# Optimization experiments

Measured on AMD Instinct MI355X. Metric: run time of the kernel, lower is better.

## Reference

```python
import jax, jax.numpy as jnp
import numpy as np

D_MODEL, D_FF, R, N_ADAPTERS = 1024, 4096, 8, 4


def setup_inputs() -> dict:
    key = jax.random.key(0)
    ks = jax.random.split(key, 8)
    s1 = 1.0 / np.sqrt(D_MODEL)
    s2 = 1.0 / np.sqrt(D_FF)
    x = jax.random.normal(ks[0], (4, 4096, D_MODEL), dtype=jnp.float32)
    w1 = jax.random.uniform(ks[1], (D_MODEL, D_FF), jnp.float32, -s1, s1)
    b1 = jax.random.uniform(ks[2], (D_FF,), jnp.float32, -s1, s1)
    w2 = jax.random.uniform(ks[3], (D_FF, D_MODEL), jnp.float32, -s2, s2)
    b2 = jax.random.uniform(ks[4], (D_MODEL,), jnp.float32, -s2, s2)
    # stacked adapters: down [A, d_model, r], up [A, r, d_model] (no bias)
    a_down = jax.random.uniform(ks[5], (N_ADAPTERS, D_MODEL, R), jnp.float32, -s1, s1)
    a_up = jax.random.uniform(ks[6], (N_ADAPTERS, R, D_MODEL), jnp.float32, -1.0 / np.sqrt(R), 1.0 / np.sqrt(R))
    return {"x": x, "w1": w1, "b1": b1, "w2": w2, "b2": b2,
            "a_down": a_down, "a_up": a_up, "adapter_idx": 0}


def reference(x, w1, b1, w2, b2, a_down, a_up, adapter_idx):
    # FFN: gelu(x @ w1 + b1) @ w2 + b2  (torch F.gelu default = exact erf form)
    h = jax.nn.gelu(jnp.einsum('bsd,df->bsf', x, w1) + b1, approximate=False)
    out = jnp.einsum('bsf,fd->bsd', h, w2) + b2
    # low-rank adapter residual: (x @ A_down) @ A_up
    lora = jnp.einsum('bsd,dr->bsr', x, a_down[adapter_idx])
    out = out + jnp.einsum('bsr,rd->bsd', lora, a_up[adapter_idx])
    return out
```

## Files before the change

### kernel.cpp

```cpp
#include <hip/hip_runtime.h>
#include <hip/hip_bf16.h>
#include <math.h>

typedef __attribute__((ext_vector_type(4))) float floatx4;
typedef __attribute__((ext_vector_type(8))) __bf16 bfloatx8;
typedef __attribute__((ext_vector_type(8))) unsigned short ushortx8;

static __device__ __forceinline__ unsigned short f2bf(float f) {
  __hip_bfloat16 h = __float2bfloat16(f);
  return *reinterpret_cast<unsigned short*>(&h);
}

static __device__ __forceinline__ void gload16(const void* g, void* l) {
  __builtin_amdgcn_global_load_lds(
      (const __attribute__((address_space(1))) unsigned int*)g,
      (__attribute__((address_space(3))) unsigned int*)l, 16, 0, 0);
}

#define S_BARRIER() __builtin_amdgcn_s_barrier()
#define WAIT_VM(n)  do { asm volatile("s_waitcnt vmcnt(" #n ")" ::: "memory"); __builtin_amdgcn_sched_barrier(0); } while (0)

__global__ __launch_bounds__(256) void transpose_bf16_kernel(const float* __restrict__ in,
                                                             unsigned short* __restrict__ out,
                                                             int rows, int cols) {
  __shared__ float tile[32][33];
  int c0 = blockIdx.x * 32, r0 = blockIdx.y * 32;
  int tx = threadIdx.x, ty = threadIdx.y;
#pragma unroll
  for (int j = 0; j < 32; j += 8)
    tile[ty + j][tx] = in[(size_t)(r0 + ty + j) * cols + c0 + tx];
  __syncthreads();
#pragma unroll
  for (int j = 0; j < 32; j += 8)
    out[(size_t)(c0 + ty + j) * rows + r0 + tx] = f2bf(tile[tx][ty + j]);
}

__global__ __launch_bounds__(256) void lora_mid_convert_kernel(const float* __restrict__ x,
                                                               const float* __restrict__ a_down,
                                                               const int* __restrict__ idxp,
                                                               float* __restrict__ lmid,
                                                               unsigned short* __restrict__ Xb) {
  __shared__ float ad[1024 * 9];
  const float* A = a_down + (size_t)(*idxp) * (1024 * 8);
  int t = threadIdx.x;
  for (int i = t; i < 2048; i += 256) {
    float4 v = ((const float4*)A)[i];
    int row = i >> 1, p = (i & 1) * 4;
    ad[row * 9 + p] = v.x; ad[row * 9 + p + 1] = v.y;
    ad[row * 9 + p + 2] = v.z; ad[row * 9 + p + 3] = v.w;
  }
  __syncthreads();
  int wid = t >> 6, lane = t & 63;
  int row = blockIdx.x * 4 + wid;
  const float4* xr4 = (const float4*)(x + (size_t)row * 1024);
  ushort4* xbr4 = (ushort4*)(Xb + (size_t)row * 1024);
  float acc[8] = {0.f, 0.f, 0.f, 0.f, 0.f, 0.f, 0.f, 0.f};
#pragma unroll
  for (int c = 0; c < 4; ++c) {
    int i4 = c * 64 + lane;
    float4 xv = xr4[i4];
    ushort4 o;
    o.x = f2bf(xv.x); o.y = f2bf(xv.y); o.z = f2bf(xv.z); o.w = f2bf(xv.w);
    xbr4[i4] = o;
    const int kb = i4 * 4;
    const float xs[4] = {xv.x, xv.y, xv.z, xv.w};
#pragma unroll
    for (int j = 0; j < 4; ++j)
#pragma unroll
      for (int r = 0; r < 8; ++r) acc[r] += xs[j] * ad[(kb + j) * 9 + r];
  }
#pragma unroll
  for (int off = 32; off > 0; off >>= 1) {
#pragma unroll
    for (int r = 0; r < 8; ++r) acc[r] += __shfl_xor(acc[r], off);
  }
  if (lane == 0) {
    *(float4*)(lmid + (size_t)row * 8) = make_float4(acc[0], acc[1], acc[2], acc[3]);
    *(float4*)(lmid + (size_t)row * 8 + 4) = make_float4(acc[4], acc[5], acc[6], acc[7]);
  }
}

template <int LD, int NKT>
static __device__ __forceinline__ void gemm_kloop3(const unsigned short* __restrict__ A,
                                                   const unsigned short* __restrict__ B,
                                                   size_t m0, size_t n0, char* smem,
                                                   floatx4 (&acc)[4][4]) {
  const int t = threadIdx.x;
  const int wid = t >> 6, lane = t & 63;
  const int wr = wid >> 1, wc = wid & 1;
  const int lr = lane & 15, kg = lane >> 4;
  const int kgx = kg ^ ((lr >> 1) & 3);
  const int srow = t >> 2, scol = ((t & 3) ^ ((t >> 3) & 3)) * 8;
  const unsigned short* gA0 = A + (m0 + srow) * LD + scol;
  const unsigned short* gA1 = A + (m0 + 64 + srow) * LD + scol;
  const unsigned short* gB0 = B + (n0 + srow) * LD + scol;
  const unsigned short* gB1 = B + (n0 + 64 + srow) * LD + scol;
  const unsigned ldsOff = (unsigned)(wid << 10);

#define STAGE(bufb, ko)                           \
  do {                                            \
    char* lA_ = smem + (bufb) + ldsOff;           \
    char* lB_ = smem + (bufb) + 8192 + ldsOff;    \
    gload16(gA0 + (ko), lA_);                     \
    gload16(gA1 + (ko), lA_ + 4096);              \
    gload16(gB0 + (ko), lB_);                     \
    gload16(gB1 + (ko), lB_ + 4096);              \
  } while (0)

  STAGE(0u, 0);
  STAGE(16384u, 32);
  WAIT_VM(4);
  S_BARRIER();

  unsigned cur = 0u, stg = 32768u;
#pragma unroll 1
  for (int kt = 0; kt < NKT; ++kt) {
    if (kt + 2 < NKT) STAGE(stg, (kt + 2) * 32);
    const unsigned short* As = (const unsigned short*)(smem + cur);
    const unsigned short* Bs = (const unsigned short*)(smem + cur + 8192);
    bfloatx8 af[4], bfv[4];
#pragma unroll
    for (int mi = 0; mi < 4; ++mi)
      af[mi] = *(const bfloatx8*)(As + (wr * 64 + mi * 16 + lr) * 32 + kgx * 8);
#pragma unroll
    for (int ni = 0; ni < 4; ++ni)
      bfv[ni] = *(const bfloatx8*)(Bs + (wc * 64 + ni * 16 + lr) * 32 + kgx * 8);
#pragma unroll
    for (int mi = 0; mi < 4; ++mi) {
#pragma unroll
      for (int ni = 0; ni < 4; ++ni)
        acc[mi][ni] = __builtin_amdgcn_mfma_f32_16x16x32_bf16(af[mi], bfv[ni], acc[mi][ni], 0, 0, 0);
    }
    if (kt + 2 < NKT) { WAIT_VM(4); } else { WAIT_VM(0); }
    S_BARRIER();
    cur = (cur == 32768u) ? 0u : cur + 16384u;
    stg = (stg == 32768u) ? 0u : stg + 16384u;
  }
#undef STAGE
}

__global__ __launch_bounds__(256, 3) void gemm1_gelu_kernel(const unsigned short* __restrict__ A,
                                                            const unsigned short* __restrict__ B,
                                                            const float* __restrict__ bias,
                                                            unsigned short* __restrict__ H) {
  __shared__ __align__(16) char smem[49152];
  const int t = threadIdx.x;
  const int wid = t >> 6, lane = t & 63;
  const int wr = wid >> 1, wc = wid & 1;
  const int lr = lane & 15, kg = lane >> 4;

  const int bid = blockIdx.x;
  const int xcd = bid & 7, j = bid >> 3;
  const int sq = j >> 6, i = j & 63;
  const int mt = xcd * 16 + (sq & 1) * 8 + (i & 7);
  const int nt = (sq >> 1) * 8 + (i >> 3);
  const size_t m0 = (size_t)mt * 128;
  const size_t n0 = (size_t)nt * 128;

  floatx4 acc[4][4] = {};
  gemm_kloop3<1024, 32>(A, B, m0, n0, smem, acc);

  __syncthreads();
  float* sE = (float*)smem;
  const int row32 = t >> 3, col0 = (t & 7) * 16;
  const int stripe = row32 >> 4, lrow = row32 & 15;
#pragma unroll
  for (int mi = 0; mi < 4; ++mi) {
#pragma unroll
    for (int ni = 0; ni < 4; ++ni) {
#pragma unroll
      for (int r = 0; r < 4; ++r)
        sE[wr * 2048 + (kg * 4 + r) * 128 + wc * 64 + ni * 16 + lr] = acc[mi][ni][r];
    }
    __syncthreads();
    const size_t gm = m0 + stripe * 64 + mi * 16 + lrow;
    const float* src = sE + stripe * 2048 + lrow * 128 + col0;
    alignas(16) unsigned short pk[16];
#pragma unroll
    for (int i2 = 0; i2 < 16; ++i2) {
      float v = src[i2] + bias[n0 + col0 + i2];
      float g = 0.5f * v * (1.0f + erff(v * 0.70710678118654752440f));
      pk[i2] = f2bf(g);
    }
    *(ushortx8*)(H + gm * 4096 + n0 + col0) = *(const ushortx8*)&pk[0];
    *(ushortx8*)(H + gm * 4096 + n0 + col0 + 8) = *(const ushortx8*)&pk[8];
    __syncthreads();
  }
}

__global__ __launch_bounds__(512) void gemm2_out_kernel(const unsigned short* __restrict__ A,
                                                        const unsigned short* __restrict__ B,
                                                        const float* __restrict__ bias,
                                                        const float* __restrict__ lmid,
                                                        const float* __restrict__ a_up,
                                                        const int* __restrict__ idxp,
                                                        float* __restrict__ OUT) {
  extern __shared__ char smem[];
  const int t = threadIdx.x;
  const int w = t >> 6, lane = t & 63, lr = lane & 15, kg = lane >> 4;
  const int kgx = kg ^ ((lr >> 1) & 3);
  constexpr int LD = 4096, NKT = 128;

  const int bid = blockIdx.x;
  const int xcd = bid & 7, j = bid >> 3;
  const size_t m0 = (size_t)(xcd * 8 + (j >> 3)) * 256;
  const size_t n0 = (size_t)(j & 7) * 128;

  const int sr = w * 16 + (lane >> 2);
  const int scol = ((t & 3) ^ ((sr >> 1) & 3)) * 8;
  const unsigned short* gA0 = A + (m0 + sr) * LD + scol;
  const unsigned short* gA1 = A + (m0 + 128 + sr) * LD + scol;
  const unsigned short* gB = B + (n0 + sr) * LD + scol;
  const unsigned wOff = (unsigned)(w << 10);

#define STAGE2(bufb, ko)                              \
  do {                                                \
    gload16(gA0 + (ko), smem + (bufb) + wOff);        \
    gload16(gA1 + (ko), smem + (bufb) + 8192 + wOff); \
    gload16(gB + (ko), smem + (bufb) + 16384 + wOff); \
  } while (0)

  floatx4 acc[2][8] = {};

  STAGE2(0u, 0);
  STAGE2(24576u, 32);
  WAIT_VM(3);
  S_BARRIER();

  unsigned cur = 0u, stg = 49152u;
#pragma unroll 1
  for (int kt = 0; kt < NKT; ++kt) {
    if (kt + 2 < NKT) STAGE2(stg, (kt + 2) * 32);
    const unsigned short* As = (const unsigned short*)(smem + cur);
    const unsigned short* Bs = (const unsigned short*)(smem + cur + 16384);
    bfloatx8 af[2];
#pragma unroll
    for (int mi = 0; mi < 2; ++mi)
      af[mi] = *(const bfloatx8*)(As + (unsigned)(w * 32 + mi * 16 + lr) * 32 + (unsigned)kgx * 8);
    {
      bfloatx8 bfA[4];
#pragma unroll
      for (int ni = 0; ni < 4; ++ni)
        bfA[ni] = *(const bfloatx8*)(Bs + (unsigned)(ni * 16 + lr) * 32 + (unsigned)kgx * 8);
#pragma unroll
      for (int mi = 0; mi < 2; ++mi)
#pragma unroll
        for (int ni = 0; ni < 4; ++ni)
          acc[mi][ni] = __builtin_amdgcn_mfma_f32_16x16x32_bf16(af[mi], bfA[ni], acc[mi][ni], 0, 0, 0);
    }
    {
      bfloatx8 bfB[4];
#pragma unroll
      for (int ni = 0; ni < 4; ++ni)
        bfB[ni] = *(const bfloatx8*)(Bs + (unsigned)((ni + 4) * 16 + lr) * 32 + (unsigned)kgx * 8);
#pragma unroll
      for (int mi = 0; mi < 2; ++mi)
#pragma unroll
        for (int ni = 0; ni < 4; ++ni)
          acc[mi][4 + ni] = __builtin_amdgcn_mfma_f32_16x16x32_bf16(af[mi], bfB[ni], acc[mi][4 + ni], 0, 0, 0);
    }
    if (kt + 2 < NKT) { WAIT_VM(3); } else { WAIT_VM(0); }
    S_BARRIER();
    cur = (cur == 49152u) ? 0u : cur + 24576u;
    stg = (stg == 49152u) ? 0u : stg + 24576u;
  }
#undef STAGE2

  __syncthreads();
  float* sE = (float*)smem;
  const float* aup = a_up + (size_t)(*idxp) * 8192;
  const int erow = t >> 3, ec0 = (t & 7) * 16;
#pragma unroll
  for (int mi = 0; mi < 2; ++mi) {
#pragma unroll
    for (int ni = 0; ni < 8; ++ni)
#pragma unroll
      for (int r = 0; r < 4; ++r)
        sE[(w * 16 + kg * 4 + r) * 128 + ni * 16 + lr] = acc[mi][ni][r];
    __syncthreads();
#pragma unroll
    for (int h = 0; h < 2; ++h) {
      const int row = erow + h * 64;
      const size_t gm = m0 + (size_t)(row >> 4) * 32 + mi * 16 + (row & 15);
      const int gc = (int)n0 + ec0;
      const float* src = sE + row * 128 + ec0;
      alignas(16) float lmv[8];
      *(float4*)&lmv[0] = *(const float4*)(lmid + gm * 8);
      *(float4*)&lmv[4] = *(const float4*)(lmid + gm * 8 + 4);
      alignas(16) float v[16];
#pragma unroll
      for (int i2 = 0; i2 < 16; ++i2) v[i2] = src[i2] + bias[gc + i2];
#pragma unroll
      for (int r = 0; r < 8; ++r) {
        const float lw = lmv[r];
        const float* ar = aup + r * 1024 + gc;
#pragma unroll
        for (int i2 = 0; i2 < 16; ++i2) v[i2] += lw * ar[i2];
      }
#pragma unroll
      for (int i2 = 0; i2 < 16; i2 += 4)
        *(float4*)(OUT + gm * 1024 + gc + i2) = *(const float4*)&v[i2];
    }
    __syncthreads();
  }
}

extern "C" void kernel_launch(void* const* d_in, const int* in_sizes, int n_in,
                              void* d_out, int out_size, void* d_ws, size_t ws_size,
                              hipStream_t stream) {
  const float* x      = (const float*)d_in[0];
  const float* w1     = (const float*)d_in[1];
  const float* b1     = (const float*)d_in[2];
  const float* w2     = (const float*)d_in[3];
  const float* b2     = (const float*)d_in[4];
  const float* a_down = (const float*)d_in[5];
  const float* a_up   = (const float*)d_in[6];
  const int*   idx    = (const int*)d_in[7];
  float* out = (float*)d_out;

  char* ws = (char*)d_ws;
  unsigned short* Xb  = (unsigned short*)(ws);
  unsigned short* W1T = (unsigned short*)(ws + 33554432);
  unsigned short* W2T = (unsigned short*)(ws + 41943040);
  float*          LMID = (float*)(ws + 50331648);
  unsigned short* H   = (unsigned short*)(ws + 50855936);

  (void)hipFuncSetAttribute((const void*)gemm2_out_kernel, hipFuncAttributeMaxDynamicSharedMemorySize, 73728);

  transpose_bf16_kernel<<<dim3(128, 32), dim3(32, 8), 0, stream>>>(w1, W1T, 1024, 4096);
  transpose_bf16_kernel<<<dim3(32, 128), dim3(32, 8), 0, stream>>>(w2, W2T, 4096, 1024);
  lora_mid_convert_kernel<<<4096, 256, 0, stream>>>(x, a_down, idx, LMID, Xb);
  gemm1_gelu_kernel<<<4096, 256, 0, stream>>>(Xb, W1T, b1, H);
  gemm2_out_kernel<<<512, 512, 73728, stream>>>(H, W2T, b2, LMID, a_up, idx, out);
}
```

Baseline: 441.3 us.

## Enlarge GEMM1 tile to 256x128 with 512 threads and 8 waves

The first GEMM goes from 128x128 tiles with 256 threads and 48KB static LDS to 256x128 tiles with 512 threads (8 waves, each owning 32 rows by 128 columns) and 72KB dynamic LDS in a triple-buffered pipeline. The grid halves to 2048 blocks and the bias+GELU epilogue is remapped to the new layout. The aim is more operand reuse per LDS byte and fewer B-tile loads from global memory. In exchange, register pressure rises and occupancy falls, since fewer blocks fit per CU.

```diff
diff --git a/kernel.cpp b/kernel.cpp
--- a/kernel.cpp
+++ b/kernel.cpp
@@ -80,110 +80,110 @@
   }
 }
 
-template <int LD, int NKT>
-static __device__ __forceinline__ void gemm_kloop3(const unsigned short* __restrict__ A,
-                                                   const unsigned short* __restrict__ B,
-                                                   size_t m0, size_t n0, char* smem,
-                                                   floatx4 (&acc)[4][4]) {
+
+__global__ __launch_bounds__(512) void gemm1_gelu_kernel(const unsigned short* __restrict__ A,
+                                                         const unsigned short* __restrict__ B,
+                                                         const float* __restrict__ bias,
+                                                         unsigned short* __restrict__ H) {
+  extern __shared__ char smem[];
   const int t = threadIdx.x;
-  const int wid = t >> 6, lane = t & 63;
-  const int wr = wid >> 1, wc = wid & 1;
-  const int lr = lane & 15, kg = lane >> 4;
+  const int w = t >> 6, lane = t & 63, lr = lane & 15, kg = lane >> 4;
   const int kgx = kg ^ ((lr >> 1) & 3);
-  const int srow = t >> 2, scol = ((t & 3) ^ ((t >> 3) & 3)) * 8;
-  const unsigned short* gA0 = A + (m0 + srow) * LD + scol;
-  const unsigned short* gA1 = A + (m0 + 64 + srow) * LD + scol;
-  const unsigned short* gB0 = B + (n0 + srow) * LD + scol;
-  const unsigned short* gB1 = B + (n0 + 64 + srow) * LD + scol;
-  const unsigned ldsOff = (unsigned)(wid << 10);
-
-#define STAGE(bufb, ko)                           \
-  do {                                            \
-    char* lA_ = smem + (bufb) + ldsOff;           \
-    char* lB_ = smem + (bufb) + 8192 + ldsOff;    \
-    gload16(gA0 + (ko), lA_);                     \
-    gload16(gA1 + (ko), lA_ + 4096);              \
-    gload16(gB0 + (ko), lB_);                     \
-    gload16(gB1 + (ko), lB_ + 4096);              \
-  } while (0)
-
-  STAGE(0u, 0);
-  STAGE(16384u, 32);
-  WAIT_VM(4);
-  S_BARRIER();
-
-  unsigned cur = 0u, stg = 32768u;
-#pragma unroll 1
-  for (int kt = 0; kt < NKT; ++kt) {
-    if (kt + 2 < NKT) STAGE(stg, (kt + 2) * 32);
-    const unsigned short* As = (const unsigned short*)(smem + cur);
-    const unsigned short* Bs = (const unsigned short*)(smem + cur + 8192);
-    bfloatx8 af[4], bfv[4];
-#pragma unroll
-    for (int mi = 0; mi < 4; ++mi)
-      af[mi] = *(const bfloatx8*)(As + (wr * 64 + mi * 16 + lr) * 32 + kgx * 8);
-#pragma unroll
-    for (int ni = 0; ni < 4; ++ni)
-      bfv[ni] = *(const bfloatx8*)(Bs + (wc * 64 + ni * 16 + lr) * 32 + kgx * 8);
-#pragma unroll
-    for (int mi = 0; mi < 4; ++mi) {
-#pragma unroll
-      for (int ni = 0; ni < 4; ++ni)
-        acc[mi][ni] = __builtin_amdgcn_mfma_f32_16x16x32_bf16(af[mi], bfv[ni], acc[mi][ni], 0, 0, 0);
-    }
-    if (kt + 2 < NKT) { WAIT_VM(4); } else { WAIT_VM(0); }
-    S_BARRIER();
-    cur = (cur == 32768u) ? 0u : cur + 16384u;
-    stg = (stg == 32768u) ? 0u : stg + 16384u;
-  }
-#undef STAGE
-}
-
-__global__ __launch_bounds__(256, 3) void gemm1_gelu_kernel(const unsigned short* __restrict__ A,
-                                                            const unsigned short* __restrict__ B,
-                                                            const float* __restrict__ bias,
-                                                            unsigned short* __restrict__ H) {
-  __shared__ __align__(16) char smem[49152];
-  const int t = threadIdx.x;
-  const int wid = t >> 6, lane = t & 63;
-  const int wr = wid >> 1, wc = wid & 1;
-  const int lr = lane & 15, kg = lane >> 4;
+  constexpr int LD = 1024, NKT = 32;
 
   const int bid = blockIdx.x;
   const int xcd = bid & 7, j = bid >> 3;
   const int sq = j >> 6, i = j & 63;
-  const int mt = xcd * 16 + (sq & 1) * 8 + (i & 7);
-  const int nt = (sq >> 1) * 8 + (i >> 3);
-  const size_t m0 = (size_t)mt * 128;
-  const size_t n0 = (size_t)nt * 128;
-
-  floatx4 acc[4][4] = {};
-  gemm_kloop3<1024, 32>(A, B, m0, n0, smem, acc);
+  const size_t m0 = (size_t)(xcd * 8 + (i & 7)) * 256;
+  const size_t n0 = (size_t)(sq * 8 + (i >> 3)) * 128;
+
+  const int sr = w * 16 + (lane >> 2);
+  const int scol = ((t & 3) ^ ((sr >> 1) & 3)) * 8;
+  const unsigned short* gA0 = A + (m0 + sr) * LD + scol;
+  const unsigned short* gA1 = A + (m0 + 128 + sr) * LD + scol;
+  const unsigned short* gB = B + (n0 + sr) * LD + scol;
+  const unsigned wOff = (unsigned)(w << 10);
+
+#define STAGE1(bufb, ko)                              \
+  do {                                                \
+    gload16(gA0 + (ko), smem + (bufb) + wOff);        \
+    gload16(gA1 + (ko), smem + (bufb) + 8192 + wOff); \
+    gload16(gB + (ko), smem + (bufb) + 16384 + wOff); \
+  } while (0)
+
+  floatx4 acc[2][8] = {};
+
+  STAGE1(0u, 0);
+  STAGE1(24576u, 32);
+  WAIT_VM(3);
+  S_BARRIER();
+
+  unsigned cur = 0u, stg = 49152u;
+#pragma unroll 1
+  for (int kt = 0; kt < NKT; ++kt) {
+    if (kt + 2 < NKT) STAGE1(stg, (kt + 2) * 32);
+    const unsigned short* As = (const unsigned short*)(smem + cur);
+    const unsigned short* Bs = (const unsigned short*)(smem + cur + 16384);
+    bfloatx8 af[2];
+#pragma unroll
+    for (int mi = 0; mi < 2; ++mi)
+      af[mi] = *(const bfloatx8*)(As + (unsigned)(w * 32 + mi * 16 + lr) * 32 + (unsigned)kgx * 8);
+    {
+      bfloatx8 bfA[4];
+#pragma unroll
+      for (int ni = 0; ni < 4; ++ni)
+        bfA[ni] = *(const bfloatx8*)(Bs + (unsigned)(ni * 16 + lr) * 32 + (unsigned)kgx * 8);
+#pragma unroll
+      for (int mi = 0; mi < 2; ++mi)
+#pragma unroll
+        for (int ni = 0; ni < 4; ++ni)
+          acc[mi][ni] = __builtin_amdgcn_mfma_f32_16x16x32_bf16(af[mi], bfA[ni], acc[mi][ni], 0, 0, 0);
+    }
+    {
+      bfloatx8 bfB[4];
+#pragma unroll
+      for (int ni = 0; ni < 4; ++ni)
+        bfB[ni] = *(const bfloatx8*)(Bs + (unsigned)((ni + 4) * 16 + lr) * 32 + (unsigned)kgx * 8);
+#pragma unroll
+      for (int mi = 0; mi < 2; ++mi)
+#pragma unroll
+        for (int ni = 0; ni < 4; ++ni)
+          acc[mi][4 + ni] = __builtin_amdgcn_mfma_f32_16x16x32_bf16(af[mi], bfB[ni], acc[mi][4 + ni], 0, 0, 0);
+    }
+    if (kt + 2 < NKT) { WAIT_VM(3); } else { WAIT_VM(0); }
+    S_BARRIER();
+    cur = (cur == 49152u) ? 0u : cur + 24576u;
+    stg = (stg == 49152u) ? 0u : stg + 24576u;
+  }
+#undef STAGE1
 
   __syncthreads();
   float* sE = (float*)smem;
-  const int row32 = t >> 3, col0 = (t & 7) * 16;
-  const int stripe = row32 >> 4, lrow = row32 & 15;
-#pragma unroll
-  for (int mi = 0; mi < 4; ++mi) {
-#pragma unroll
-    for (int ni = 0; ni < 4; ++ni) {
+  const int erow = t >> 3, ec0 = (t & 7) * 16;
+#pragma unroll
+  for (int mi = 0; mi < 2; ++mi) {
+#pragma unroll
+    for (int ni = 0; ni < 8; ++ni)
 #pragma unroll
       for (int r = 0; r < 4; ++r)
-        sE[wr * 2048 + (kg * 4 + r) * 128 + wc * 64 + ni * 16 + lr] = acc[mi][ni][r];
-    }
+        sE[(w * 16 + kg * 4 + r) * 128 + ni * 16 + lr] = acc[mi][ni][r];
     __syncthreads();
-    const size_t gm = m0 + stripe * 64 + mi * 16 + lrow;
-    const float* src = sE + stripe * 2048 + lrow * 128 + col0;
-    alignas(16) unsigned short pk[16];
-#pragma unroll
-    for (int i2 = 0; i2 < 16; ++i2) {
-      float v = src[i2] + bias[n0 + col0 + i2];
-      float g = 0.5f * v * (1.0f + erff(v * 0.70710678118654752440f));
-      pk[i2] = f2bf(g);
-    }
-    *(ushortx8*)(H + gm * 4096 + n0 + col0) = *(const ushortx8*)&pk[0];
-    *(ushortx8*)(H + gm * 4096 + n0 + col0 + 8) = *(const ushortx8*)&pk[8];
+#pragma unroll
+    for (int h = 0; h < 2; ++h) {
+      const int row = erow + h * 64;
+      const size_t gm = m0 + (size_t)(row >> 4) * 32 + mi * 16 + (row & 15);
+      const int gc = (int)n0 + ec0;
+      const float* src = sE + row * 128 + ec0;
+      alignas(16) unsigned short pk[16];
+#pragma unroll
+      for (int i2 = 0; i2 < 16; ++i2) {
+        float v = src[i2] + bias[gc + i2];
+        float g = 0.5f * v * (1.0f + erff(v * 0.70710678118654752440f));
+        pk[i2] = f2bf(g);
+      }
+      *(ushortx8*)(H + gm * 4096 + gc) = *(const ushortx8*)&pk[0];
+      *(ushortx8*)(H + gm * 4096 + gc + 8) = *(const ushortx8*)&pk[8];
+    }
     __syncthreads();
   }
 }
@@ -325,11 +325,12 @@
   float*          LMID = (float*)(ws + 50331648);
   unsigned short* H   = (unsigned short*)(ws + 50855936);
 
+  (void)hipFuncSetAttribute((const void*)gemm1_gelu_kernel, hipFuncAttributeMaxDynamicSharedMemorySize, 73728);
   (void)hipFuncSetAttribute((const void*)gemm2_out_kernel, hipFuncAttributeMaxDynamicSharedMemorySize, 73728);
 
   transpose_bf16_kernel<<<dim3(128, 32), dim3(32, 8), 0, stream>>>(w1, W1T, 1024, 4096);
   transpose_bf16_kernel<<<dim3(32, 128), dim3(32, 8), 0, stream>>>(w2, W2T, 4096, 1024);
   lora_mid_convert_kernel<<<4096, 256, 0, stream>>>(x, a_down, idx, LMID, Xb);
-  gemm1_gelu_kernel<<<4096, 256, 0, stream>>>(Xb, W1T, b1, H);
+  gemm1_gelu_kernel<<<2048, 512, 73728, stream>>>(Xb, W1T, b1, H);
   gemm2_out_kernel<<<512, 512, 73728, stream>>>(H, W2T, b2, LMID, a_up, idx, out);
 }
```

Measured after the change: 432.8 us. Within noise of the previous version (-1.9%).
